# Kernel tuning notes

Measured on AMD Instinct MI355X. Metric: run time of the kernel, lower is better.

The kernel has to match this reference:

```python
import jax, jax.numpy as jnp
import numpy as np

NUM_CODES = 8192
BETA = 0.25


def setup_inputs() -> dict:
    key = jax.random.key(0)
    k1, k2 = jax.random.split(key)
    z_e = jax.random.normal(k1, (8, 64, 64, 64), dtype=jnp.float32)  # (B, D, H, W)
    embedding = jax.random.normal(k2, (NUM_CODES, 64), dtype=jnp.float32) * 0.01  # (K, D)
    return {"z_e": z_e, "embedding": embedding}


def reference(z_e, embedding):
    b, d, h, w = z_e.shape
    # (B, D, H, W) -> (B*H*W, D)
    z_flat = jnp.transpose(z_e, (0, 2, 3, 1)).reshape(-1, d)
    zf = jax.lax.stop_gradient(z_flat)  # lookup uses z_flat.detach()

    # pairwise squared distances: |a|^2 - 2 a.b + |b|^2
    a2 = jnp.sum(zf * zf, axis=1, keepdims=True)           # (N, 1)
    b2 = jnp.sum(embedding * embedding, axis=1)            # (K,)
    ab = zf @ embedding.T                                  # (N, K) GEMM, inner dim D
    dist = a2 - 2.0 * ab + b2[None, :]
    idx = jnp.argmin(dist, axis=1)                         # (N,)
    q_flat = embedding[idx]                                # (N, D) gather

    # straight-through estimator
    z_q_flat = z_flat + jax.lax.stop_gradient(q_flat - z_flat)
    commit_loss = BETA * jnp.mean((z_flat - jax.lax.stop_gradient(q_flat)) ** 2)

    # usage / perplexity stats (no-grad in original)
    counts = jnp.zeros((NUM_CODES,), z_e.dtype).at[idx].add(1.0)
    avg = counts / idx.shape[0]
    perplexity = jnp.exp(-jnp.sum(avg * jnp.log(avg + 1e-10)))
    usage = jnp.mean((counts > 0).astype(z_e.dtype))

    z_q = jnp.transpose(z_q_flat.reshape(b, h, w, d), (0, 3, 1, 2))  # (B, D, H, W)
    indices = idx.reshape(b, h, w)
    return z_q, indices, commit_loss, perplexity, usage
```

## Files before the change

### kernel.cpp

```cpp
#include <hip/hip_runtime.h>


#define K_CODES   8192
#define DIMV      64
#define IDX_OFF   2097152
#define SCAL_OFF  2129920
#define MARGIN    1e-4f

#define WS_B2    0
#define WS_IDX   32768
#define WS_CNT   163840
#define WS_LOSS  196608
#define WS_FCNT  196612
#define WS_FLIST 196672
#define WS_A2    327744
#define WS_EFRAG 458816
#define WS_ZHI   2555968
#define WS_ZLO   6750272
#define WS_P1V   10944576
#define WS_P2V   11468864
#define WS_P1I   11993152

typedef short s16x8  __attribute__((ext_vector_type(8)));
typedef float f32x4  __attribute__((ext_vector_type(4)));

__device__ __forceinline__ short bf16rne(float x) {
    unsigned u = __float_as_uint(x);
    unsigned r = (u + 0x7FFFu + ((u >> 16) & 1u)) >> 16;
    return (short)r;
}
__device__ __forceinline__ float bf16tof(short s) {
    return __uint_as_float(((unsigned)(unsigned short)s) << 16);
}

__device__ __forceinline__ void gl_lds16(const char* g, char* l) {
    __builtin_amdgcn_global_load_lds(
        (const __attribute__((address_space(1))) unsigned int*)g,
        (__attribute__((address_space(3))) unsigned int*)l, 16, 0, 0);
}

__device__ __forceinline__ float pairwise8_sq(const float* __restrict__ x) {
    float r[8];
#pragma unroll
    for (int j = 0; j < 8; ++j) r[j] = __fmul_rn(x[j], x[j]);
#pragma unroll
    for (int i = 8; i < 64; i += 8)
#pragma unroll
        for (int j = 0; j < 8; ++j)
            r[j] = __fadd_rn(r[j], __fmul_rn(x[i + j], x[i + j]));
    const float s01 = __fadd_rn(r[0], r[1]);
    const float s23 = __fadd_rn(r[2], r[3]);
    const float s45 = __fadd_rn(r[4], r[5]);
    const float s67 = __fadd_rn(r[6], r[7]);
    return __fadd_rn(__fadd_rn(s01, s23), __fadd_rn(s45, s67));
}

__global__ __launch_bounds__(256)
void vq_prep(const float* __restrict__ z_e, const float* __restrict__ emb,
             float* __restrict__ a2, float* __restrict__ b2,
             short* __restrict__ zt_hi, short* __restrict__ zt_lo,
             short* __restrict__ efrag, int* __restrict__ zero_base) {
    const int blk = blockIdx.x;
    const int tid = threadIdx.x;
    if (blk < 512) {
        __shared__ float zs[64][65];
        const int b = blk >> 6, h = blk & 63;
        {
            const int w = tid & 63, dq = tid >> 6;
#pragma unroll
            for (int i = 0; i < 16; ++i) {
                const int dd = dq + i * 4;
                zs[w][dd] = z_e[((b * 64 + dd) << 12) + (h << 6) + w];
            }
        }
        __syncthreads();
        if (tid < 64) {
            float v[64];
#pragma unroll
            for (int d = 0; d < 64; ++d) v[d] = zs[tid][d];
            a2[blk * 64 + tid] = pairwise8_sq(v);
        }
        const int w = tid & 63, dq = tid >> 6;
        const int n = blk * 64 + w;
        s16x8 h8[2], l8[2];
#pragma unroll
        for (int i = 0; i < 16; ++i) {
            const float x = zs[w][dq * 16 + i];
            const short hh = bf16rne(x);
            ((short*)h8)[i] = hh;
            ((short*)l8)[i] = bf16rne(x - bf16tof(hh));
        }
        *(s16x8*)(zt_hi + n * DIMV + dq * 16)     = h8[0];
        *(s16x8*)(zt_hi + n * DIMV + dq * 16 + 8) = h8[1];
        *(s16x8*)(zt_lo + n * DIMV + dq * 16)     = l8[0];
        *(s16x8*)(zt_lo + n * DIMV + dq * 16 + 8) = l8[1];
    } else {
        const int zi = (blk - 512) * 256 + tid;
        if (zi < 8194) zero_base[zi] = 0;
        if (tid < 128) {
            const int k = (blk - 512) * 128 + tid;
            float v[64];
            const float4* row = (const float4*)(emb + k * DIMV);
#pragma unroll
            for (int i = 0; i < 16; ++i) {
                const float4 q = row[i];
                v[i*4+0] = q.x; v[i*4+1] = q.y; v[i*4+2] = q.z; v[i*4+3] = q.w;
            }
            b2[k] = pairwise8_sq(v);
            const int c = k >> 6, ct = (k >> 4) & 3, lcol = k & 15;
#pragma unroll
            for (int g = 0; g < 8; ++g) {
                s16x8 hv, lv;
#pragma unroll
                for (int j = 0; j < 8; ++j) {
                    const float x = -2.0f * v[g*8 + j];
                    const short hh = bf16rne(x);
                    hv[j] = hh;
                    lv[j] = bf16rne(x - bf16tof(hh));
                }
                const int f  = ct*4 + (g >> 2)*2;
                const int ln = (g & 3)*16 + lcol;
                *(s16x8*)(efrag + c*8192 + f*512     + ln*8) = hv;
                *(s16x8*)(efrag + c*8192 + (f+1)*512 + ln*8) = lv;
            }
        }
    }
}

__global__ __launch_bounds__(256, 4)
void vq_argmin_mfma(const short* __restrict__ zt_hi, const short* __restrict__ zt_lo,
                    const short* __restrict__ efrag, const float* __restrict__ b2,
                    float* __restrict__ p_b1v, float* __restrict__ p_b2v,
                    int* __restrict__ p_b1i) {
    __shared__ __align__(16) char lds[2][16384];
    const int tid  = threadIdx.x;
    const int lane = tid & 63;
    const int wid  = tid >> 6;
    const int blk  = blockIdx.x;
    const int quar = blk & 3;
    const int rgrp = blk >> 2;
    const int n0   = rgrp * 128 + wid * 32;
    const int lcol = lane & 15;
    const int kq   = lane >> 4;

    s16x8 a_h[2][2], a_l[2][2];
#pragma unroll
    for (int rt = 0; rt < 2; ++rt) {
        const short* zh = zt_hi + (size_t)(n0 + rt*16 + lcol) * DIMV + kq*8;
        const short* zl = zt_lo + (size_t)(n0 + rt*16 + lcol) * DIMV + kq*8;
        a_h[rt][0] = *(const s16x8*)(zh);
        a_h[rt][1] = *(const s16x8*)(zh + 32);
        a_l[rt][0] = *(const s16x8*)(zl);
        a_l[rt][1] = *(const s16x8*)(zl + 32);
    }

    float b1v[2][4], b2v[2][4]; int b1i[2][4];
#pragma unroll
    for (int rt = 0; rt < 2; ++rt)
#pragma unroll
        for (int r = 0; r < 4; ++r) { b1v[rt][r] = 3.4e38f; b2v[rt][r] = 3.4e38f; b1i[rt][r] = 0; }

    const int c0 = quar * 32;
    const char* gbase = (const char*)efrag;

    {
        const char* src = gbase + (size_t)c0 * 16384 + tid * 16;
        char* dst = &lds[0][tid * 16];
#pragma unroll
        for (int i = 0; i < 4; ++i) gl_lds16(src + i * 4096, dst + i * 4096);
    }

    for (int t = 0; t < 32; ++t) {
        __syncthreads();
        if (t < 31) {
            const char* src = gbase + (size_t)(c0 + t + 1) * 16384 + tid * 16;
            char* dst = &lds[(t + 1) & 1][tid * 16];
#pragma unroll
            for (int i = 0; i < 4; ++i) gl_lds16(src + i * 4096, dst + i * 4096);
        }
        const char* base = lds[t & 1];
        s16x8 B[16];
#pragma unroll
        for (int f = 0; f < 16; ++f)
            B[f] = *(const s16x8*)(base + f*1024 + lane*16);

        const int kt = (c0 + t) * 64;
        float b2f[4];
#pragma unroll
        for (int ct = 0; ct < 4; ++ct) b2f[ct] = b2[kt + ct*16 + lcol];

#pragma unroll
        for (int ct = 0; ct < 4; ++ct) {
            const int code = kt + ct*16 + lcol;
#pragma unroll
            for (int rt = 0; rt < 2; ++rt) {
                f32x4 acc = {b2f[ct], b2f[ct], b2f[ct], b2f[ct]};
                acc = __builtin_amdgcn_mfma_f32_16x16x32_bf16(a_h[rt][0], B[ct*4+0], acc, 0, 0, 0);
                acc = __builtin_amdgcn_mfma_f32_16x16x32_bf16(a_h[rt][1], B[ct*4+2], acc, 0, 0, 0);
                acc = __builtin_amdgcn_mfma_f32_16x16x32_bf16(a_l[rt][0], B[ct*4+0], acc, 0, 0, 0);
                acc = __builtin_amdgcn_mfma_f32_16x16x32_bf16(a_l[rt][1], B[ct*4+2], acc, 0, 0, 0);
                acc = __builtin_amdgcn_mfma_f32_16x16x32_bf16(a_h[rt][0], B[ct*4+1], acc, 0, 0, 0);
                acc = __builtin_amdgcn_mfma_f32_16x16x32_bf16(a_h[rt][1], B[ct*4+3], acc, 0, 0, 0);
#pragma unroll
                for (int r = 0; r < 4; ++r) {
                    const float v = acc[r];
                    b2v[rt][r] = __builtin_amdgcn_fmed3f(v, b1v[rt][r], b2v[rt][r]);
                    const bool lt = (v < b1v[rt][r]);
                    b1i[rt][r] = lt ? code : b1i[rt][r];
                    b1v[rt][r] = fminf(v, b1v[rt][r]);
                }
            }
        }
    }

#pragma unroll
    for (int m = 8; m >= 1; m >>= 1) {
#pragma unroll
        for (int rt = 0; rt < 2; ++rt)
#pragma unroll
            for (int r = 0; r < 4; ++r) {
                const float ov1 = __shfl_xor(b1v[rt][r], m);
                const int   oi1 = __shfl_xor(b1i[rt][r], m);
                const float ov2 = __shfl_xor(b2v[rt][r], m);
                const bool take = (ov1 < b1v[rt][r]) || (ov1 == b1v[rt][r] && oi1 < b1i[rt][r]);
                const float nb2 = take ? fminf(b1v[rt][r], ov2) : fminf(b2v[rt][r], ov1);
                if (take) { b1v[rt][r] = ov1; b1i[rt][r] = oi1; }
                b2v[rt][r] = nb2;
            }
    }
    if (lcol == 0) {
#pragma unroll
        for (int rt = 0; rt < 2; ++rt)
#pragma unroll
            for (int r = 0; r < 4; ++r) {
                const int n = n0 + rt*16 + kq*4 + r;
                p_b1v[quar * 32768 + n] = b1v[rt][r];
                p_b2v[quar * 32768 + n] = b2v[rt][r];
                p_b1i[quar * 32768 + n] = b1i[rt][r];
            }
    }
}

__global__ __launch_bounds__(256)
void vq_merge(const float* __restrict__ p_b1v, const float* __restrict__ p_b2v,
              const int* __restrict__ p_b1i, int* __restrict__ idx_out,
              float* __restrict__ out, int* __restrict__ counts,
              int* __restrict__ fcnt, int* __restrict__ flist) {
    const int n = blockIdx.x * 256 + threadIdx.x;
    float b1 = p_b1v[n], sec = p_b2v[n];
    int   bi = p_b1i[n];
#pragma unroll
    for (int q = 1; q < 4; ++q) {
        const float v = p_b1v[q * 32768 + n];
        const float s = p_b2v[q * 32768 + n];
        const int   i = p_b1i[q * 32768 + n];
        const bool take = (v < b1);
        sec = take ? fminf(b1, s) : fminf(sec, v);
        b1  = take ? v : b1;
        bi  = take ? i : bi;
    }
    idx_out[n] = bi;
    out[IDX_OFF + n] = (float)bi;
    atomicAdd(&counts[bi], 1);
    if (sec - b1 < MARGIN) {
        const int p = atomicAdd(fcnt, 1);
        flist[p] = n;
    }
}

__global__ __launch_bounds__(256)
void vq_refine1(const float* __restrict__ z_e, const float* __restrict__ emb,
                const float* __restrict__ a2, const float* __restrict__ b2,
                const int* __restrict__ fcnt, const int* __restrict__ flist,
                float* __restrict__ pq_v, int* __restrict__ pq_i) {
    __shared__ float  es[128][65];
    __shared__ float  zsh[64];
    __shared__ double pd[128];
    __shared__ float  bv[128];
    __shared__ int    bix[128];
    const int tid = threadIdx.x;
    const int cnt = *fcnt;
    const int njobs = cnt * 4;
    const int c  = tid & 127;
    const int hh = tid >> 7;
    const int dh = hh * 32;

    for (int j = blockIdx.x; j < njobs; j += gridDim.x) {
        const int it = j >> 2, q = j & 3;
        const int n  = flist[it];
        const int b = n >> 12, h = (n >> 6) & 63, w = n & 63;
        __syncthreads();
        if (tid < 64) zsh[tid] = z_e[(((b << 6) + tid) << 12) + (h << 6) + w];
        __syncthreads();

        float zreg[32];
#pragma unroll
        for (int i = 0; i < 32; ++i) zreg[i] = zsh[dh + i];
        const float a2n = a2[n];

        float best = 3.4e38f;
        int   bi   = 0;
        const int kbase = q * 2048;

        for (int t = 0; t < 16; ++t) {
            const int kt = kbase + t * 128;
            __syncthreads();
#pragma unroll
            for (int i = 0; i < 8; ++i) {
                const int g  = i * 256 + tid;
                const int cc = g >> 4, dd = (g & 15) * 4;
                const float4 v = *(const float4*)(emb + (size_t)(kt + cc) * DIMV + dd);
                es[cc][dd + 0] = v.x; es[cc][dd + 1] = v.y;
                es[cc][dd + 2] = v.z; es[cc][dd + 3] = v.w;
            }
            __syncthreads();

            double s0 = 0.0, s1 = 0.0, s2 = 0.0, s3 = 0.0;
#pragma unroll
            for (int i = 0; i < 32; i += 4) {
                s0 += (double)zreg[i + 0] * (double)es[c][dh + i + 0];
                s1 += (double)zreg[i + 1] * (double)es[c][dh + i + 1];
                s2 += (double)zreg[i + 2] * (double)es[c][dh + i + 2];
                s3 += (double)zreg[i + 3] * (double)es[c][dh + i + 3];
            }
            const double sh = (s0 + s1) + (s2 + s3);
            if (hh == 1) pd[c] = sh;
            __syncthreads();
            if (hh == 0) {
                const double full = sh + pd[c];
                const float qab  = (float)full;
                const float m2ab = __fmul_rn(-2.0f, qab);
                const float t1   = __fadd_rn(a2n, m2ab);
                const float dist = __fadd_rn(t1, b2[kt + c]);
                if (dist < best) { best = dist; bi = kt + c; }
            }
        }

        if (hh == 0) { bv[c] = best; bix[c] = bi; }
        __syncthreads();
#pragma unroll
        for (int s = 64; s > 0; s >>= 1) {
            if (tid < s) {
                const float ov = bv[tid + s];
                const int   oi = bix[tid + s];
                if (ov < bv[tid] || (ov == bv[tid] && oi < bix[tid])) { bv[tid] = ov; bix[tid] = oi; }
            }
            __syncthreads();
        }
        if (tid == 0) { pq_v[q * 32768 + n] = bv[0]; pq_i[q * 32768 + n] = bix[0]; }
    }
}

__global__ __launch_bounds__(256)
void vq_refine2(const float* __restrict__ pq_v, const int* __restrict__ pq_i,
                const int* __restrict__ fcnt, const int* __restrict__ flist,
                int* __restrict__ idx_out, float* __restrict__ out,
                int* __restrict__ counts) {
    const int cnt = *fcnt;
    for (int i = blockIdx.x * 256 + threadIdx.x; i < cnt; i += gridDim.x * 256) {
        const int n = flist[i];
        float best = pq_v[n];
        int   bi   = pq_i[n];
#pragma unroll
        for (int q = 1; q < 4; ++q) {
            const float v = pq_v[q * 32768 + n];
            if (v < best) { best = v; bi = pq_i[q * 32768 + n]; }
        }
        const int oldbi = idx_out[n];
        if (bi != oldbi) {
            idx_out[n] = bi;
            out[IDX_OFF + n] = (float)bi;
            atomicSub(&counts[oldbi], 1);
            atomicAdd(&counts[bi], 1);
        }
    }
}

__global__ __launch_bounds__(256)
void vq_quant(const float* __restrict__ z_e, const float* __restrict__ emb,
              const int* __restrict__ idx, float* __restrict__ out,
              float* __restrict__ loss_acc) {
    __shared__ float q[64][65];
    const int tid = threadIdx.x;
    const int tile = blockIdx.x;
    const int b = tile >> 6, h = tile & 63;
    {
        const int r = tid >> 2, qd = (tid & 3) * 16;
        const int code = idx[tile * 64 + r];
        const float4* er = (const float4*)(emb + code * DIMV + qd);
#pragma unroll
        for (int i = 0; i < 4; ++i) {
            const float4 e4 = er[i];
            q[r][qd + i*4 + 0] = e4.x;
            q[r][qd + i*4 + 1] = e4.y;
            q[r][qd + i*4 + 2] = e4.z;
            q[r][qd + i*4 + 3] = e4.w;
        }
    }
    __syncthreads();
    const int w = tid & 63, dq = tid >> 6;
    float dl = 0.f;
#pragma unroll
    for (int i = 0; i < 16; ++i) {
        const int d = dq * 16 + i;
        const int g = ((b * 64 + d) << 12) + (h << 6) + w;
        const float qq = q[w][d];
        const float zz = z_e[g];
        out[g] = qq;
        const float df = zz - qq;
        dl = fmaf(df, df, dl);
    }
    __shared__ float red[256];
    red[tid] = dl;
    __syncthreads();
#pragma unroll
    for (int s = 128; s > 0; s >>= 1) {
        if (tid < s) red[tid] += red[tid + s];
        __syncthreads();
    }
    if (tid == 0) atomicAdd(loss_acc, red[0]);
}

__global__ __launch_bounds__(256)
void vq_stats_kernel(const int* __restrict__ counts, const float* __restrict__ loss_acc,
                     float* __restrict__ out) {
    __shared__ float rent[256];
    __shared__ float ruse[256];
    float ent = 0.f, used = 0.f;
    for (int k = threadIdx.x; k < K_CODES; k += 256) {
        const int c = counts[k];
        if (c > 0) {
            const float avg = (float)c * (1.0f / 32768.0f);
            ent  += avg * logf(avg + 1e-10f);
            used += 1.0f;
        }
    }
    rent[threadIdx.x] = ent;
    ruse[threadIdx.x] = used;
    __syncthreads();
#pragma unroll
    for (int s = 128; s > 0; s >>= 1) {
        if (threadIdx.x < s) {
            rent[threadIdx.x] += rent[threadIdx.x + s];
            ruse[threadIdx.x] += ruse[threadIdx.x + s];
        }
        __syncthreads();
    }
    if (threadIdx.x == 0) {
        out[SCAL_OFF + 0] = 0.25f * loss_acc[0] * (1.0f / 2097152.0f);
        out[SCAL_OFF + 1] = expf(-rent[0]);
        out[SCAL_OFF + 2] = ruse[0] * (1.0f / 8192.0f);
    }
}

extern "C" void kernel_launch(void* const* d_in, const int* in_sizes, int n_in,
                              void* d_out, int out_size, void* d_ws, size_t ws_size,
                              hipStream_t stream) {
    const float* z_e = (const float*)d_in[0];
    const float* emb = (const float*)d_in[1];
    float* out = (float*)d_out;
    char*  ws  = (char*)d_ws;

    float* b2     = (float*)(ws + WS_B2);
    int*   idx    = (int*)(ws + WS_IDX);
    int*   counts = (int*)(ws + WS_CNT);
    float* loss   = (float*)(ws + WS_LOSS);
    int*   fcnt   = (int*)(ws + WS_FCNT);
    int*   flist  = (int*)(ws + WS_FLIST);
    float* a2     = (float*)(ws + WS_A2);
    short* efrag  = (short*)(ws + WS_EFRAG);
    short* zt_hi  = (short*)(ws + WS_ZHI);
    short* zt_lo  = (short*)(ws + WS_ZLO);
    float* p_b1v  = (float*)(ws + WS_P1V);
    float* p_b2v  = (float*)(ws + WS_P2V);
    int*   p_b1i  = (int*)(ws + WS_P1I);

    hipLaunchKernelGGL(vq_prep,        dim3(576),  dim3(256), 0, stream,
                       z_e, emb, a2, b2, zt_hi, zt_lo, efrag, counts);
    hipLaunchKernelGGL(vq_argmin_mfma, dim3(1024), dim3(256), 0, stream,
                       zt_hi, zt_lo, efrag, b2, p_b1v, p_b2v, p_b1i);
    hipLaunchKernelGGL(vq_merge,       dim3(128),  dim3(256), 0, stream,
                       p_b1v, p_b2v, p_b1i, idx, out, counts, fcnt, flist);
    hipLaunchKernelGGL(vq_refine1,     dim3(1024), dim3(256), 0, stream,
                       z_e, emb, a2, b2, fcnt, flist, p_b1v, p_b1i);
    hipLaunchKernelGGL(vq_refine2,     dim3(64),   dim3(256), 0, stream,
                       p_b1v, p_b1i, fcnt, flist, idx, out, counts);
    hipLaunchKernelGGL(vq_quant,       dim3(512),  dim3(256), 0, stream,
                       z_e, emb, idx, out, loss);
    hipLaunchKernelGGL(vq_stats_kernel, dim3(1),   dim3(256), 0, stream, counts, loss, out);
}
```

Before: 224.8 us.

## Fuse merge into argmin and stats into quant via last-block counters

Folds the partial-result merge into the argmin kernel: the last of the four column-quarter blocks for each row group, found with an atomic counter, does the merge. The per-row statistics go into the quantize kernel the same way, with a global done counter. The a2 precompute moves into refine1, and refine2 becomes a flag-driven patch kernel that reads a per-row flag stored over p_b2v. This cuts the kernel count from seven to five, removing launch gaps, at the cost of extra atomics and threadfences. It also leaves dead placeholder code in vq_quant.

```diff
diff --git a/kernel.cpp b/kernel.cpp
--- a/kernel.cpp
+++ b/kernel.cpp
@@ -12,8 +12,9 @@
 #define WS_CNT   163840
 #define WS_LOSS  196608
 #define WS_FCNT  196612
+#define WS_DONE  196616
 #define WS_FLIST 196672
-#define WS_A2    327744
+#define WS_RGRP  327744
 #define WS_EFRAG 458816
 #define WS_ZHI   2555968
 #define WS_ZLO   6750272
@@ -32,13 +33,11 @@
 __device__ __forceinline__ float bf16tof(short s) {
     return __uint_as_float(((unsigned)(unsigned short)s) << 16);
 }
-
 __device__ __forceinline__ void gl_lds16(const char* g, char* l) {
     __builtin_amdgcn_global_load_lds(
         (const __attribute__((address_space(1))) unsigned int*)g,
         (__attribute__((address_space(3))) unsigned int*)l, 16, 0, 0);
 }
-
 __device__ __forceinline__ float pairwise8_sq(const float* __restrict__ x) {
     float r[8];
 #pragma unroll
@@ -57,9 +56,9 @@
 
 __global__ __launch_bounds__(256)
 void vq_prep(const float* __restrict__ z_e, const float* __restrict__ emb,
-             float* __restrict__ a2, float* __restrict__ b2,
-             short* __restrict__ zt_hi, short* __restrict__ zt_lo,
-             short* __restrict__ efrag, int* __restrict__ zero_base) {
+             float* __restrict__ b2, short* __restrict__ zt_hi,
+             short* __restrict__ zt_lo, short* __restrict__ efrag,
+             int* __restrict__ zero_base, int* __restrict__ rgrp_ctr) {
     const int blk = blockIdx.x;
     const int tid = threadIdx.x;
     if (blk < 512) {
@@ -74,12 +73,6 @@
             }
         }
         __syncthreads();
-        if (tid < 64) {
-            float v[64];
-#pragma unroll
-            for (int d = 0; d < 64; ++d) v[d] = zs[tid][d];
-            a2[blk * 64 + tid] = pairwise8_sq(v);
-        }
         const int w = tid & 63, dq = tid >> 6;
         const int n = blk * 64 + w;
         s16x8 h8[2], l8[2];
@@ -96,7 +89,8 @@
         *(s16x8*)(zt_lo + n * DIMV + dq * 16 + 8) = l8[1];
     } else {
         const int zi = (blk - 512) * 256 + tid;
-        if (zi < 8194) zero_base[zi] = 0;
+        if (zi < 8195) zero_base[zi] = 0;
+        if (blk == 575 && tid < 256) rgrp_ctr[tid] = 0;
         if (tid < 128) {
             const int k = (blk - 512) * 128 + tid;
             float v[64];
@@ -131,8 +125,12 @@
 void vq_argmin_mfma(const short* __restrict__ zt_hi, const short* __restrict__ zt_lo,
                     const short* __restrict__ efrag, const float* __restrict__ b2,
                     float* __restrict__ p_b1v, float* __restrict__ p_b2v,
-                    int* __restrict__ p_b1i) {
+                    int* __restrict__ p_b1i, int* __restrict__ rgrp_ctr,
+                    int* __restrict__ idx, float* __restrict__ out,
+                    int* __restrict__ counts, int* __restrict__ fcnt,
+                    int* __restrict__ flist) {
     __shared__ __align__(16) char lds[2][16384];
+    __shared__ int amLast;
     const int tid  = threadIdx.x;
     const int lane = tid & 63;
     const int wid  = tid >> 6;
@@ -162,7 +160,6 @@
 
     const int c0 = quar * 32;
     const char* gbase = (const char*)efrag;
-
     {
         const char* src = gbase + (size_t)c0 * 16384 + tid * 16;
         char* dst = &lds[0][tid * 16];
@@ -239,39 +236,44 @@
                 p_b1i[quar * 32768 + n] = b1i[rt][r];
             }
     }
-}
-
-__global__ __launch_bounds__(256)
-void vq_merge(const float* __restrict__ p_b1v, const float* __restrict__ p_b2v,
-              const int* __restrict__ p_b1i, int* __restrict__ idx_out,
-              float* __restrict__ out, int* __restrict__ counts,
-              int* __restrict__ fcnt, int* __restrict__ flist) {
-    const int n = blockIdx.x * 256 + threadIdx.x;
-    float b1 = p_b1v[n], sec = p_b2v[n];
-    int   bi = p_b1i[n];
-#pragma unroll
-    for (int q = 1; q < 4; ++q) {
-        const float v = p_b1v[q * 32768 + n];
-        const float s = p_b2v[q * 32768 + n];
-        const int   i = p_b1i[q * 32768 + n];
-        const bool take = (v < b1);
-        sec = take ? fminf(b1, s) : fminf(sec, v);
-        b1  = take ? v : b1;
-        bi  = take ? i : bi;
-    }
-    idx_out[n] = bi;
-    out[IDX_OFF + n] = (float)bi;
-    atomicAdd(&counts[bi], 1);
-    if (sec - b1 < MARGIN) {
-        const int p = atomicAdd(fcnt, 1);
-        flist[p] = n;
+
+    __threadfence();
+    __syncthreads();
+    if (tid == 0) amLast = (atomicAdd(&rgrp_ctr[rgrp], 1) == 3) ? 1 : 0;
+    __syncthreads();
+    if (amLast) {
+        __threadfence();
+        if (tid < 128) {
+            const int n = rgrp * 128 + tid;
+            float b1 = p_b1v[n], sec = p_b2v[n];
+            int   bi = p_b1i[n];
+#pragma unroll
+            for (int q = 1; q < 4; ++q) {
+                const float v = p_b1v[q * 32768 + n];
+                const float s = p_b2v[q * 32768 + n];
+                const int   i = p_b1i[q * 32768 + n];
+                const bool take = (v < b1);
+                sec = take ? fminf(b1, s) : fminf(sec, v);
+                b1  = take ? v : b1;
+                bi  = take ? i : bi;
+            }
+            idx[n] = bi;
+            out[IDX_OFF + n] = (float)bi;
+            atomicAdd(&counts[bi], 1);
+            const int fl = (sec - b1 < MARGIN) ? 1 : 0;
+            ((int*)p_b2v)[n] = fl;
+            if (fl) {
+                const int p = atomicAdd(fcnt, 1);
+                flist[p] = n;
+            }
+        }
     }
 }
 
 __global__ __launch_bounds__(256)
 void vq_refine1(const float* __restrict__ z_e, const float* __restrict__ emb,
-                const float* __restrict__ a2, const float* __restrict__ b2,
-                const int* __restrict__ fcnt, const int* __restrict__ flist,
+                const float* __restrict__ b2, const int* __restrict__ fcnt,
+                const int* __restrict__ flist,
                 float* __restrict__ pq_v, int* __restrict__ pq_i) {
     __shared__ float  es[128][65];
     __shared__ float  zsh[64];
@@ -293,15 +295,14 @@
         if (tid < 64) zsh[tid] = z_e[(((b << 6) + tid) << 12) + (h << 6) + w];
         __syncthreads();
 
+        const float a2n = pairwise8_sq(zsh);
         float zreg[32];
 #pragma unroll
         for (int i = 0; i < 32; ++i) zreg[i] = zsh[dh + i];
-        const float a2n = a2[n];
 
         float best = 3.4e38f;
         int   bi   = 0;
         const int kbase = q * 2048;
-
         for (int t = 0; t < 16; ++t) {
             const int kt = kbase + t * 128;
             __syncthreads();
@@ -335,7 +336,6 @@
                 if (dist < best) { best = dist; bi = kt + c; }
             }
         }
-
         if (hh == 0) { bv[c] = best; bix[c] = bi; }
         __syncthreads();
 #pragma unroll
@@ -352,41 +352,32 @@
 }
 
 __global__ __launch_bounds__(256)
-void vq_refine2(const float* __restrict__ pq_v, const int* __restrict__ pq_i,
-                const int* __restrict__ fcnt, const int* __restrict__ flist,
-                int* __restrict__ idx_out, float* __restrict__ out,
-                int* __restrict__ counts) {
-    const int cnt = *fcnt;
-    for (int i = blockIdx.x * 256 + threadIdx.x; i < cnt; i += gridDim.x * 256) {
-        const int n = flist[i];
-        float best = pq_v[n];
-        int   bi   = pq_i[n];
-#pragma unroll
-        for (int q = 1; q < 4; ++q) {
-            const float v = pq_v[q * 32768 + n];
-            if (v < best) { best = v; bi = pq_i[q * 32768 + n]; }
-        }
-        const int oldbi = idx_out[n];
-        if (bi != oldbi) {
-            idx_out[n] = bi;
-            out[IDX_OFF + n] = (float)bi;
-            atomicSub(&counts[oldbi], 1);
-            atomicAdd(&counts[bi], 1);
-        }
-    }
-}
-
-__global__ __launch_bounds__(256)
 void vq_quant(const float* __restrict__ z_e, const float* __restrict__ emb,
-              const int* __restrict__ idx, float* __restrict__ out,
-              float* __restrict__ loss_acc) {
+              int* __restrict__ idx, const float* __restrict__ pq_v,
+              const int* __restrict__ pq_i, float* __restrict__ out,
+              int* __restrict__ counts, float* __restrict__ loss,
+              int* __restrict__ done_ctr) {
     __shared__ float q[64][65];
+    __shared__ float red[256];
+    __shared__ float ruse[256];
+    __shared__ int amLast;
     const int tid = threadIdx.x;
-    const int tile = blockIdx.x;
-    const int b = tile >> 6, h = tile & 63;
+    const int blk = blockIdx.x;
+    const int b = blk >> 6, h = blk & 63;
+
+    if (tid < 64) {
+        const int n = blk * 64 + tid;
+        if (((const int*)pq_v)[32768 * 0 + 0 == 0 ? n : n]) {  }
+        const int fl = ((const int*)(pq_v + 32768))[n - 32768 >= 0 ? 0 : 0];
+    }
+    if (tid < 64) {
+        const int n = blk * 64 + tid;
+    }
+    __syncthreads();
+
     {
         const int r = tid >> 2, qd = (tid & 3) * 16;
-        const int code = idx[tile * 64 + r];
+        const int code = idx[blk * 64 + r];
         const float4* er = (const float4*)(emb + code * DIMV + qd);
 #pragma unroll
         for (int i = 0; i < 4; ++i) {
@@ -410,7 +401,6 @@
         const float df = zz - qq;
         dl = fmaf(df, df, dl);
     }
-    __shared__ float red[256];
     red[tid] = dl;
     __syncthreads();
 #pragma unroll
@@ -418,38 +408,64 @@
         if (tid < s) red[tid] += red[tid + s];
         __syncthreads();
     }
-    if (tid == 0) atomicAdd(loss_acc, red[0]);
+    if (tid == 0) atomicAdd(loss, red[0]);
+
+    __threadfence();
+    __syncthreads();
+    if (tid == 0) amLast = (atomicAdd(done_ctr, 1) == 511) ? 1 : 0;
+    __syncthreads();
+    if (amLast) {
+        __threadfence();
+        float* rent = (float*)q;
+        float ent = 0.f, used = 0.f;
+        for (int k = tid; k < K_CODES; k += 256) {
+            const int c = atomicAdd(&counts[k], 0);
+            if (c > 0) {
+                const float avg = (float)c * (1.0f / 32768.0f);
+                ent  += avg * logf(avg + 1e-10f);
+                used += 1.0f;
+            }
+        }
+        rent[tid] = ent;
+        ruse[tid] = used;
+        __syncthreads();
+#pragma unroll
+        for (int s = 128; s > 0; s >>= 1) {
+            if (tid < s) {
+                rent[tid] += rent[tid + s];
+                ruse[tid] += ruse[tid + s];
+            }
+            __syncthreads();
+        }
+        if (tid == 0) {
+            const float lv = atomicAdd(loss, 0.0f);
+            out[SCAL_OFF + 0] = 0.25f * lv * (1.0f / 2097152.0f);
+            out[SCAL_OFF + 1] = expf(-rent[0]);
+            out[SCAL_OFF + 2] = ruse[0] * (1.0f / 8192.0f);
+        }
+    }
 }
 
 __global__ __launch_bounds__(256)
-void vq_stats_kernel(const int* __restrict__ counts, const float* __restrict__ loss_acc,
-                     float* __restrict__ out) {
-    __shared__ float rent[256];
-    __shared__ float ruse[256];
-    float ent = 0.f, used = 0.f;
-    for (int k = threadIdx.x; k < K_CODES; k += 256) {
-        const int c = counts[k];
-        if (c > 0) {
-            const float avg = (float)c * (1.0f / 32768.0f);
-            ent  += avg * logf(avg + 1e-10f);
-            used += 1.0f;
-        }
-    }
-    rent[threadIdx.x] = ent;
-    ruse[threadIdx.x] = used;
-    __syncthreads();
-#pragma unroll
-    for (int s = 128; s > 0; s >>= 1) {
-        if (threadIdx.x < s) {
-            rent[threadIdx.x] += rent[threadIdx.x + s];
-            ruse[threadIdx.x] += ruse[threadIdx.x + s];
-        }
-        __syncthreads();
-    }
-    if (threadIdx.x == 0) {
-        out[SCAL_OFF + 0] = 0.25f * loss_acc[0] * (1.0f / 2097152.0f);
-        out[SCAL_OFF + 1] = expf(-rent[0]);
-        out[SCAL_OFF + 2] = ruse[0] * (1.0f / 8192.0f);
+void vq_patch(const int* __restrict__ flag, const float* __restrict__ pq_v,
+              const int* __restrict__ pq_i, int* __restrict__ idx,
+              float* __restrict__ out, int* __restrict__ counts) {
+    const int n = blockIdx.x * 256 + threadIdx.x;
+    if (n >= 32768) return;
+    if (!flag[n]) return;
+    float best = pq_v[n];
+    int   bi   = pq_i[n];
+#pragma unroll
+    for (int q2 = 1; q2 < 4; ++q2) {
+        const float v = pq_v[q2 * 32768 + n];
+        if (v < best) { best = v; bi = pq_i[q2 * 32768 + n]; }
+    }
+    const int oldbi = idx[n];
+    if (bi != oldbi) {
+        idx[n] = bi;
+        out[IDX_OFF + n] = (float)bi;
+        atomicSub(&counts[oldbi], 1);
+        atomicAdd(&counts[bi], 1);
     }
 }
 
@@ -466,26 +482,26 @@
     int*   counts = (int*)(ws + WS_CNT);
     float* loss   = (float*)(ws + WS_LOSS);
     int*   fcnt   = (int*)(ws + WS_FCNT);
+    int*   done   = (int*)(ws + WS_DONE);
     int*   flist  = (int*)(ws + WS_FLIST);
-    float* a2     = (float*)(ws + WS_A2);
+    int*   rgrp   = (int*)(ws + WS_RGRP);
     short* efrag  = (short*)(ws + WS_EFRAG);
     short* zt_hi  = (short*)(ws + WS_ZHI);
     short* zt_lo  = (short*)(ws + WS_ZLO);
     float* p_b1v  = (float*)(ws + WS_P1V);
     float* p_b2v  = (float*)(ws + WS_P2V);
     int*   p_b1i  = (int*)(ws + WS_P1I);
+    int*   flag   = (int*)(ws + WS_P2V);
 
     hipLaunchKernelGGL(vq_prep,        dim3(576),  dim3(256), 0, stream,
-                       z_e, emb, a2, b2, zt_hi, zt_lo, efrag, counts);
+                       z_e, emb, b2, zt_hi, zt_lo, efrag, counts, rgrp);
     hipLaunchKernelGGL(vq_argmin_mfma, dim3(1024), dim3(256), 0, stream,
-                       zt_hi, zt_lo, efrag, b2, p_b1v, p_b2v, p_b1i);
-    hipLaunchKernelGGL(vq_merge,       dim3(128),  dim3(256), 0, stream,
-                       p_b1v, p_b2v, p_b1i, idx, out, counts, fcnt, flist);
+                       zt_hi, zt_lo, efrag, b2, p_b1v, p_b2v, p_b1i,
+                       rgrp, idx, out, counts, fcnt, flist);
     hipLaunchKernelGGL(vq_refine1,     dim3(1024), dim3(256), 0, stream,
-                       z_e, emb, a2, b2, fcnt, flist, p_b1v, p_b1i);
-    hipLaunchKernelGGL(vq_refine2,     dim3(64),   dim3(256), 0, stream,
-                       p_b1v, p_b1i, fcnt, flist, idx, out, counts);
+                       z_e, emb, b2, fcnt, flist, p_b1v, p_b1i);
+    hipLaunchKernelGGL(vq_patch,       dim3(128),  dim3(256), 0, stream,
+                       flag, p_b1v, p_b1i, idx, out, counts);
     hipLaunchKernelGGL(vq_quant,       dim3(512),  dim3(256), 0, stream,
-                       z_e, emb, idx, out, loss);
-    hipLaunchKernelGGL(vq_stats_kernel, dim3(1),   dim3(256), 0, stream, counts, loss, out);
-}
+                       z_e, emb, idx, p_b1v, p_b1i, out, counts, loss, done);
+}
```

After: 349.2 us. +55.3%, slower.
